# Optimization experiments

Hardware: AMD Instinct MI355X
Metric: run time of the kernel (lower is better)

The kernel has to match this reference:

```python
import jax, jax.numpy as jnp
import numpy as np

# Module hyperparameters (match init_kwargs)
T0, Z0, T1, Z1, K, S, ROUTING = 4, 16, 8, 16, 5, 1, 3
PAD = 2  # hard-coded padding=2 in the torch module
N, H, W_SP = 4, 128, 128


def setup_inputs() -> dict:
    key = jax.random.key(0)
    k1, k2 = jax.random.split(key)
    u = jax.random.normal(k1, (N, T0, Z0, H, W_SP), dtype=jnp.float32)
    # t_0 independent Conv2d(z_0 -> t_1*z_1, k, s, padding=2, bias=False) weights
    W = jax.random.normal(k2, (T0, T1 * Z1, Z0, K, K), dtype=jnp.float32) * 0.05
    return {"u": u, "W": W}


def _squash(p):
    # squash along last (z_1) axis, matching torch: p_norm = sqrt(|p|^2 + 1e-9)
    n2 = jnp.sum(p * p, axis=-1, keepdims=True)
    n = jnp.sqrt(n2 + 1e-9)
    return n2 / (1.0 + n2) * p / n


def _capsule_convs(u, W):
    # t_0 independent convs == one grouped conv with feature_group_count=t_0
    n, t0, z0, h, w = u.shape
    x = u.reshape(n, t0 * z0, h, w)
    wk = W.reshape(t0 * T1 * Z1, z0, K, K)
    y = jax.lax.conv_general_dilated(
        x, wk, window_strides=(S, S), padding=[(PAD, PAD), (PAD, PAD)],
        dimension_numbers=("NCHW", "OIHW", "NCHW"), feature_group_count=t0)
    h1, w1 = y.shape[2], y.shape[3]
    # [N, t0*t1*z1, H1, W1] -> u_hat [t0, N, H1, W1, t1, z1]
    y = y.reshape(n, t0, T1, Z1, h1, w1)
    return jnp.transpose(y, (1, 0, 4, 5, 2, 3))


def _routing(u_hat):
    t0, n, h, w, t1, z1 = u_hat.shape
    dt = u_hat.dtype
    b = jnp.zeros((t0, n, t1, h, w), dt)  # NCHW layout per capsule type
    neg_inf = jnp.array(-jnp.inf, dt)
    zero = jnp.array(0.0, dt)
    win = (1, 1, 1, K, K)
    ones = (1, 1, 1, 1, 1)
    pad = [(0, 0), (0, 0), (0, 0), (PAD, PAD), (PAD, PAD)]
    v = None
    for d in range(ROUTING):
        uh = jax.lax.stop_gradient(u_hat) if d < ROUTING - 1 else u_hat
        # stability max: max_pool2d(k,1,pad=2) (pads with -inf) then max over t1
        b_max = jax.lax.reduce_window(b, neg_inf, jax.lax.max, win, ones, pad)
        b_max = jnp.max(b_max, axis=2, keepdims=True)
        c = jnp.exp(b - b_max)  # [t0, N, t1, H, W]
        # conv2d_same with ones kernel [1,t1,k,k] == channel-sum then kxk box-sum
        sum_c = jax.lax.reduce_window(jnp.sum(c, axis=2, keepdims=True), zero,
                                      jax.lax.add, win, ones, pad)
        r = c / sum_c                                   # [t0, N, t1, H, W]
        r = jnp.transpose(r, (0, 1, 3, 4, 2))[..., None]  # [t0,N,H,W,t1,1]
        p = jnp.sum(r * uh, axis=0)                     # [N, H, W, t1, z1]
        v = _squash(p)
        # NOTE: the original torch code computes b + (u_hat*v).sum(4) into a
        # list `b_t_list_` that is never assigned back, so b stays zero across
        # iterations. We faithfully reproduce that (no b update).
    return jnp.transpose(v, (0, 3, 4, 1, 2))  # [N, t1, z1, H, W]


def reference(u, W):
    return _routing(_capsule_convs(u, W))
```

## Files before the change

kernel.cpp:

```cpp
#include <hip/hip_runtime.h>
#include <hip/hip_bf16.h>


#define CO 128

typedef __attribute__((ext_vector_type(8))) short bf16x8;
typedef __attribute__((ext_vector_type(4))) float f32x4;

__global__ __launch_bounds__(256) void k_prep(const float* __restrict__ u,
                                              const float* __restrict__ Wsrc,
                                              ushort* __restrict__ ut,
                                              ushort* __restrict__ Wr2b) {
    __shared__ float lt[64][65];
    int b = blockIdx.x;
    int t = threadIdx.x;
    if (b < 800) {
        int idx = b * 256 + t;
        int ci = idx & 63;
        int r  = idx >> 6;
        int co = r & 127;
        int kk = r >> 7;
        int t0 = ci >> 4, z0 = ci & 15;
        __hip_bfloat16 bb = __float2bfloat16(Wsrc[((t0 * CO + co) * 16 + z0) * 25 + kk]);
        int cg = co >> 6, ni = (co >> 4) & 3, m16 = co & 15;
        int ks = ci >> 5, q = (ci >> 3) & 3, j = ci & 7;
        int oi = ((((kk * 2 + cg) * 2 + ks) * 4 + ni) << 9) + ((q * 16 + m16) << 3) + j;
        Wr2b[oi] = *(ushort*)&bb;
        return;
    }
    b -= 800;
    int wc = b & 1; int nh = b >> 1; int h = nh & 127; int n = nh >> 7;
    int w0 = wc * 64;
    int ciL = t >> 4;
    int wl  = (t & 15) * 4;
    const float* up = u + (size_t)n * (64 * 128 * 128) + h * 128 + w0;
#pragma unroll
    for (int p = 0; p < 4; ++p) {
        int ci = p * 16 + ciL;
        float4 v = *(const float4*)(up + (size_t)ci * 16384 + wl);
        lt[wl + 0][ci] = v.x;
        lt[wl + 1][ci] = v.y;
        lt[wl + 2][ci] = v.z;
        lt[wl + 3][ci] = v.w;
    }
    __syncthreads();
    ushort* op = ut + (((size_t)(n * 128 + h)) * 128 + w0) * 64;
#pragma unroll
    for (int p = 0; p < 2; ++p) {
        int item = p * 256 + t;
        int c8 = item & 7, w2 = item >> 3;
        bf16x8 vv;
#pragma unroll
        for (int j = 0; j < 8; ++j) {
            __hip_bfloat16 bb = __float2bfloat16(lt[w2][c8 * 8 + j]);
            vv[j] = *(ushort*)&bb;
        }
        *(bf16x8*)(op + (size_t)w2 * 64 + c8 * 8) = vv;
    }
}

__global__ __launch_bounds__(256) void k_caps(const ushort* __restrict__ ut,
                                              const ushort* __restrict__ Wr2b,
                                              float* __restrict__ out) {
    __shared__ ushort As[240 * 68];

    int tid = threadIdx.x;
    int bid = blockIdx.x;
    int bx = bid & 7, by = (bid >> 3) & 15, n = bid >> 7;
    int h0 = by * 8, w0 = bx * 16;

    int lane = tid & 63, wid = tid >> 6;
    int rg = wid >> 1;
    int cg = wid & 1;
    int wm4  = rg * 4;
    int wn64 = cg * 64;
    int q = lane >> 4, m16 = lane & 15;

    const ushort* wp = Wr2b + ((size_t)cg * 4096) + lane * 8;

    bf16x8 bA[8], bB[8];
#define LOADB(dst, kk2)                                                  \
    {                                                                    \
        _Pragma("unroll") for (int ks_ = 0; ks_ < 2; ++ks_)              \
            _Pragma("unroll") for (int ni_ = 0; ni_ < 4; ++ni_)          \
                dst[ks_ * 4 + ni_] = *(const bf16x8*)(                   \
                    wp + (size_t)(kk2) * 8192 + (ks_ * 4 + ni_) * 512);  \
    }

    LOADB(bA, 0);

    for (int i = tid; i < 1920; i += 256) {
        int p = i >> 3, c = i & 7;
        int rr = p / 20, cc = p - rr * 20;
        int hh = h0 + rr - 2, ww = w0 + cc - 2;
        bf16x8 v = {};
        if (((unsigned)hh < 128u) & ((unsigned)ww < 128u))
            v = *(const bf16x8*)(ut + (((size_t)(n * 128 + hh)) * 128 + ww) * 64 + c * 8);
        *(bf16x8*)&As[p * 68 + c * 8] = v;
    }
    __syncthreads();
    LOADB(bB, 1);

    const ushort* ap = As + (wm4 * 20 + m16) * 68 + q * 8;

#define LOADA(dst, kk2)                                                     \
    {                                                                       \
        const int kh_ = (kk2) / 5, kw_ = (kk2) % 5;                         \
        _Pragma("unroll") for (int ks_ = 0; ks_ < 2; ++ks_)                 \
            _Pragma("unroll") for (int mi_ = 0; mi_ < 4; ++mi_)             \
                dst[ks_ * 4 + mi_] = *(const bf16x8*)(                      \
                    ap + ((mi_ + kh_) * 20 + kw_) * 68 + ks_ * 32);         \
    }

    bf16x8 aA[8], aB[8];
    LOADA(aA, 0);

    f32x4 acc[4][4] = {};

#pragma unroll
    for (int kk = 0; kk < 25; ++kk) {
        if (kk < 24) {
            if (kk & 1) { LOADA(aA, kk + 1); }
            else        { LOADA(aB, kk + 1); }
        }
        const bf16x8* av = (kk & 1) ? aB : aA;
        const bf16x8* bv = (kk & 1) ? bB : bA;
#pragma unroll
        for (int ks = 0; ks < 2; ++ks)
#pragma unroll
            for (int mi = 0; mi < 4; ++mi)
#pragma unroll
                for (int ni = 0; ni < 4; ++ni)
                    acc[mi][ni] = __builtin_amdgcn_mfma_f32_16x16x32_bf16(
                        av[ks * 4 + mi], bv[ks * 4 + ni], acc[mi][ni], 0, 0, 0);
        if (kk < 23) {
            if (kk & 1) { LOADB(bB, kk + 2); }
            else        { LOADB(bA, kk + 2); }
        }
    }
#undef LOADA
#undef LOADB

#pragma unroll
    for (int mi = 0; mi < 4; ++mi) {
        int h = h0 + wm4 + mi;
        int hlo = h - 2; if (hlo < 0) hlo = 0;
        int hhi = h + 2; if (hhi > 127) hhi = 127;
        float cnth = (float)(hhi - hlo + 1);
#pragma unroll
        for (int ni = 0; ni < 4; ++ni) {
            f32x4 cv = acc[mi][ni];
            float ov[4];
#pragma unroll
            for (int reg = 0; reg < 4; ++reg) {
                int w = w0 + q * 4 + reg;
                int wlo = w - 2; if (wlo < 0) wlo = 0;
                int whi = w + 2; if (whi > 127) whi = 127;
                float s = 1.f / (8.f * cnth * (float)(whi - wlo + 1));
                float pv = cv[reg] * s;
                float n2 = pv * pv;
                n2 += __shfl_xor(n2, 1);
                n2 += __shfl_xor(n2, 2);
                n2 += __shfl_xor(n2, 4);
                n2 += __shfl_xor(n2, 8);
                float fac = n2 / ((1.f + n2) * sqrtf(n2 + 1e-9f));
                ov[reg] = pv * fac;
            }
            int co = wn64 + ni * 16 + m16;
            *(float4*)(out + (((size_t)(n * CO + co)) << 14) + h * 128 + w0 + q * 4) =
                make_float4(ov[0], ov[1], ov[2], ov[3]);
        }
    }
}

extern "C" void kernel_launch(void* const* d_in, const int* in_sizes, int n_in,
                              void* d_out, int out_size, void* d_ws, size_t ws_size,
                              hipStream_t stream) {
    const float* u    = (const float*)d_in[0];
    const float* Wsrc = (const float*)d_in[1];
    float* out = (float*)d_out;
    ushort* Wr2b = (ushort*)d_ws;
    ushort* ut   = (ushort*)((char*)d_ws + 409600);

    k_prep<<<1824, 256, 0, stream>>>(u, Wsrc, ut, Wr2b);
    k_caps<<<512, 256, 0, stream>>>(ut, Wr2b, out);
}
```

Baseline: 110.1 us.

## Split output channels across 8 waves per block with finer-grained double buffering

The conv/routing kernel now runs 512 threads per block (8 waves), with each wave covering 32 output channels instead of 64. The weight layout in the prep kernel is reshuffled to match. Operand prefetch is restructured to double-buffer per k-slice, so each wave holds a quarter of the A/B fragment registers and half the accumulators. The goal is to cut register pressure and raise occupancy and latency hiding. The trade-off is more waves redundantly loading the same A tile from LDS and more per-block sync overhead.

```diff
diff --git a/kernel.cpp b/kernel.cpp
--- a/kernel.cpp
+++ b/kernel.cpp
@@ -22,9 +22,9 @@
         int kk = r >> 7;
         int t0 = ci >> 4, z0 = ci & 15;
         __hip_bfloat16 bb = __float2bfloat16(Wsrc[((t0 * CO + co) * 16 + z0) * 25 + kk]);
-        int cg = co >> 6, ni = (co >> 4) & 3, m16 = co & 15;
+        int cg = co >> 5, ni = (co >> 4) & 1, m16 = co & 15;
         int ks = ci >> 5, q = (ci >> 3) & 3, j = ci & 7;
-        int oi = ((((kk * 2 + cg) * 2 + ks) * 4 + ni) << 9) + ((q * 16 + m16) << 3) + j;
+        int oi = ((((kk * 4 + cg) * 2 + ks) * 2 + ni) << 9) + ((q * 16 + m16) << 3) + j;
         Wr2b[oi] = *(ushort*)&bb;
         return;
     }
@@ -59,9 +59,9 @@
     }
 }
 
-__global__ __launch_bounds__(256) void k_caps(const ushort* __restrict__ ut,
-                                              const ushort* __restrict__ Wr2b,
-                                              float* __restrict__ out) {
+__global__ __launch_bounds__(512, 4) void k_caps(const ushort* __restrict__ ut,
+                                                 const ushort* __restrict__ Wr2b,
+                                                 float* __restrict__ out) {
     __shared__ ushort As[240 * 68];
 
     int tid = threadIdx.x;
@@ -70,26 +70,25 @@
     int h0 = by * 8, w0 = bx * 16;
 
     int lane = tid & 63, wid = tid >> 6;
-    int rg = wid >> 1;
-    int cg = wid & 1;
+    int rg = wid >> 2;
+    int cg = wid & 3;
     int wm4  = rg * 4;
-    int wn64 = cg * 64;
+    int wn32 = cg * 32;
     int q = lane >> 4, m16 = lane & 15;
 
-    const ushort* wp = Wr2b + ((size_t)cg * 4096) + lane * 8;
+    const ushort* wp = Wr2b + ((size_t)cg * 2048) + lane * 8;
 
-    bf16x8 bA[8], bB[8];
-#define LOADB(dst, kk2)                                                  \
-    {                                                                    \
-        _Pragma("unroll") for (int ks_ = 0; ks_ < 2; ++ks_)              \
-            _Pragma("unroll") for (int ni_ = 0; ni_ < 4; ++ni_)          \
-                dst[ks_ * 4 + ni_] = *(const bf16x8*)(                   \
-                    wp + (size_t)(kk2) * 8192 + (ks_ * 4 + ni_) * 512);  \
+    bf16x8 bbuf[2][4];
+#define LOADB(par, kk2)                                                   \
+    {                                                                     \
+        _Pragma("unroll") for (int i_ = 0; i_ < 4; ++i_)                  \
+            bbuf[par][i_] = *(const bf16x8*)(                             \
+                wp + (size_t)(kk2) * 8192 + i_ * 512);                    \
     }
 
-    LOADB(bA, 0);
+    LOADB(0, 0);
 
-    for (int i = tid; i < 1920; i += 256) {
+    for (int i = tid; i < 1920; i += 512) {
         int p = i >> 3, c = i & 7;
         int rr = p / 20, cc = p - rr * 20;
         int hh = h0 + rr - 2, ww = w0 + cc - 2;
@@ -99,43 +98,36 @@
         *(bf16x8*)&As[p * 68 + c * 8] = v;
     }
     __syncthreads();
-    LOADB(bB, 1);
 
     const ushort* ap = As + (wm4 * 20 + m16) * 68 + q * 8;
 
-#define LOADA(dst, kk2)                                                     \
+    bf16x8 abuf[2][4];
+#define LOADA(par, kk2, ks2)                                                \
     {                                                                       \
         const int kh_ = (kk2) / 5, kw_ = (kk2) % 5;                         \
-        _Pragma("unroll") for (int ks_ = 0; ks_ < 2; ++ks_)                 \
-            _Pragma("unroll") for (int mi_ = 0; mi_ < 4; ++mi_)             \
-                dst[ks_ * 4 + mi_] = *(const bf16x8*)(                      \
-                    ap + ((mi_ + kh_) * 20 + kw_) * 68 + ks_ * 32);         \
+        _Pragma("unroll") for (int mi_ = 0; mi_ < 4; ++mi_)                 \
+            abuf[par][mi_] = *(const bf16x8*)(                              \
+                ap + ((mi_ + kh_) * 20 + kw_) * 68 + (ks2) * 32);           \
     }
 
-    bf16x8 aA[8], aB[8];
-    LOADA(aA, 0);
+    LOADA(0, 0, 0);
 
-    f32x4 acc[4][4] = {};
+    f32x4 acc[4][2] = {};
 
 #pragma unroll
     for (int kk = 0; kk < 25; ++kk) {
-        if (kk < 24) {
-            if (kk & 1) { LOADA(aA, kk + 1); }
-            else        { LOADA(aB, kk + 1); }
-        }
-        const bf16x8* av = (kk & 1) ? aB : aA;
-        const bf16x8* bv = (kk & 1) ? bB : bA;
 #pragma unroll
-        for (int ks = 0; ks < 2; ++ks)
+        for (int ks = 0; ks < 2; ++ks) {
+            const int h = kk * 2 + ks;
+            if (h + 1 < 50) { LOADA((h + 1) & 1, (h + 1) >> 1, (h + 1) & 1); }
+            if (ks == 0 && kk < 24) { LOADB((kk + 1) & 1, kk + 1); }
 #pragma unroll
             for (int mi = 0; mi < 4; ++mi)
 #pragma unroll
-                for (int ni = 0; ni < 4; ++ni)
+                for (int ni = 0; ni < 2; ++ni)
                     acc[mi][ni] = __builtin_amdgcn_mfma_f32_16x16x32_bf16(
-                        av[ks * 4 + mi], bv[ks * 4 + ni], acc[mi][ni], 0, 0, 0);
-        if (kk < 23) {
-            if (kk & 1) { LOADB(bB, kk + 2); }
-            else        { LOADB(bA, kk + 2); }
+                        abuf[h & 1][mi], bbuf[kk & 1][ks * 2 + ni],
+                        acc[mi][ni], 0, 0, 0);
         }
     }
 #undef LOADA
@@ -148,7 +140,7 @@
         int hhi = h + 2; if (hhi > 127) hhi = 127;
         float cnth = (float)(hhi - hlo + 1);
 #pragma unroll
-        for (int ni = 0; ni < 4; ++ni) {
+        for (int ni = 0; ni < 2; ++ni) {
             f32x4 cv = acc[mi][ni];
             float ov[4];
 #pragma unroll
@@ -166,7 +158,7 @@
                 float fac = n2 / ((1.f + n2) * sqrtf(n2 + 1e-9f));
                 ov[reg] = pv * fac;
             }
-            int co = wn64 + ni * 16 + m16;
+            int co = wn32 + ni * 16 + m16;
             *(float4*)(out + (((size_t)(n * CO + co)) << 14) + h * 128 + w0 + q * 4) =
                 make_float4(ov[0], ov[1], ov[2], ov[3]);
         }
@@ -183,5 +175,5 @@
     ushort* ut   = (ushort*)((char*)d_ws + 409600);
 
     k_prep<<<1824, 256, 0, stream>>>(u, Wsrc, ut, Wr2b);
-    k_caps<<<512, 256, 0, stream>>>(ut, Wr2b, out);
+    k_caps<<<512, 512, 0, stream>>>(ut, Wr2b, out);
 }
```

After: 149.8 us. +36.1%, slower.
